# Performance work log

Hardware: AMD Instinct MI355X
Metric: run time of the kernel (lower is better)

## Reference

```python
import jax, jax.numpy as jnp
import numpy as np

NUM_HEADS = 16
KEY_DIM = 128
VALUE_DIM = 128
HIDDEN = 2048


def setup_inputs() -> dict:
    key = jax.random.key(0)
    k1, k2, k3 = jax.random.split(key, 3)
    B, T = 4, 2048
    hidden_states = jax.random.normal(k1, (B, T, HIDDEN), dtype=jnp.float32)
    # qkv_proj: Linear(hidden, H*(2*key_dim+value_dim)) no bias -> weight (out, in)
    qkv_out = NUM_HEADS * (2 * KEY_DIM + VALUE_DIM)
    w_qkv = jax.random.normal(k2, (qkv_out, HIDDEN), dtype=jnp.float32) * (1.0 / np.sqrt(HIDDEN))
    w_out = jax.random.normal(k3, (HIDDEN, NUM_HEADS * VALUE_DIM), dtype=jnp.float32) * (1.0 / np.sqrt(NUM_HEADS * VALUE_DIM))
    b_out = jnp.zeros((HIDDEN,), dtype=jnp.float32)
    return {"hidden_states": hidden_states, "w_qkv": w_qkv, "w_out": w_out, "b_out": b_out}


def reference(hidden_states, w_qkv, w_out, b_out):
    B, T, _ = hidden_states.shape
    H, Dk, Dv = NUM_HEADS, KEY_DIM, VALUE_DIM
    scale = 1.0 / np.sqrt(Dk).astype(np.float32)
    qkv = hidden_states @ w_qkv.T  # (B,T,H*(2Dk+Dv))
    q, k, v = jnp.split(qkv, [H * Dk, 2 * H * Dk], axis=-1)
    q = q.reshape(B, T, H, Dk).transpose(0, 2, 1, 3)  # (B,H,T,Dk)
    k = k.reshape(B, T, H, Dk).transpose(0, 2, 1, 3)
    v = v.reshape(B, T, H, Dv).transpose(0, 2, 1, 3)
    scores = jnp.einsum('bhtd,bhsd->bhts', q, k) * scale  # (B,H,T,S)
    causal = jnp.tril(jnp.ones((T, T), dtype=bool))
    scores = jnp.where(causal[None, None], scores, jnp.float32(-jnp.inf))
    attn = jax.nn.softmax(scores, axis=-1)
    out = jnp.einsum('bhts,bhsd->bhtd', attn, v)  # (B,H,T,Dv)
    out = out.transpose(0, 2, 1, 3).reshape(B, T, H * Dv)
    return out @ w_out.T + b_out
```

## Files before the change

### kernel.cpp

```cpp
#include <hip/hip_runtime.h>
#include <hip/hip_bf16.h>
#include <stdint.h>

#define HID   2048
#define NH    16
#define QKV_N 6144
#define BT    8192
#define TT    2048

typedef short bf16x8  __attribute__((ext_vector_type(8)));
typedef float f32x4   __attribute__((ext_vector_type(4)));
typedef float f32x16  __attribute__((ext_vector_type(16)));
typedef unsigned short u16;

__device__ __forceinline__ u16 f2bf(float f){
  union { float f; unsigned u; } v; v.f = f;
  unsigned r = 0x7fffu + ((v.u >> 16) & 1u);
  return (u16)((v.u + r) >> 16);
}
__device__ __forceinline__ float bf2f(u16 x){
  union { unsigned u; float f; } v; v.u = ((unsigned)x) << 16;
  return v.f;
}
__device__ __forceinline__ unsigned cvt_pk_bf16(float lo, float hi){
  unsigned r;
  asm("v_cvt_pk_bf16_f32 %0, %1, %2" : "=v"(r) : "v"(lo), "v"(hi));
  return r;
}

typedef __attribute__((address_space(3))) void lds_vt;
typedef const __attribute__((address_space(1))) void gbl_vt;

__device__ __forceinline__ void gload16(const void* g, void* l){
  __builtin_amdgcn_global_load_lds((gbl_vt*)g, (lds_vt*)l, 16, 0, 0);
}

#define FENCE() asm volatile("" ::: "memory")
#define SYNC()  { FENCE(); __builtin_amdgcn_s_barrier(); FENCE(); }

__global__ __launch_bounds__(256) void cvt_all(const float* __restrict__ in1, u16* __restrict__ o1, int n1,
                                               const float* __restrict__ in2, u16* __restrict__ o2, int n2,
                                               const float* __restrict__ in3, u16* __restrict__ o3, int n3){
  int i = blockIdx.x * blockDim.x + threadIdx.x;
  const int stride = gridDim.x * blockDim.x;
  const int ntot = n1 + n2 + n3;
  for (; i < ntot; i += stride){
    const float* ip; u16* op; int k;
    if (i < n1)            { ip = in1; op = o1; k = i; }
    else if (i < n1 + n2)  { ip = in2; op = o2; k = i - n1; }
    else                   { ip = in3; op = o3; k = i - n1 - n2; }
    float4 v = ((const float4*)ip)[k];
    ushort4 o;
    o.x = f2bf(v.x); o.y = f2bf(v.y); o.z = f2bf(v.z); o.w = f2bf(v.w);
    ((ushort4*)op)[k] = o;
  }
}

template<int OUT_BF16>
__global__ __launch_bounds__(512, 2) void gemm256(const u16* __restrict__ A,
                                                  const u16* __restrict__ Bm,
                                                  u16* __restrict__ Cb,
                                                  float* __restrict__ Cf,
                                                  const float* __restrict__ bias,
                                                  int M, int N, int K)
{
  __shared__ u16 lds[4 * 256 * 64];
  u16* const Abuf[2] = { lds,          lds + 16384 };
  u16* const Bbuf[2] = { lds + 32768,  lds + 49152 };

  const int tid  = threadIdx.x;
  const int w    = tid >> 6;
  const int lane = tid & 63;
  const int wm   = w >> 2;
  const int wn   = w & 3;
  const int lr   = lane & 15;
  const int lg   = lane >> 4;

  int bid = blockIdx.x;
  { int qq = gridDim.x >> 3; bid = (bid & 7) * qq + (bid >> 3); }
  const int ntile = N >> 8;
  const int m0 = (bid / ntile) << 8;
  const int n0 = (bid % ntile) << 8;

  const int rS = tid >> 3;
  const int cS = ((tid & 7) ^ (rS & 7)) * 8;
  const u16* gA = A  + (size_t)(m0 + rS) * K + cS;
  const u16* gB = Bm + (size_t)(n0 + rS) * K + cS;
  const int wds = w * 512;

  f32x4 acc[8][4] = {};
  bf16x8 aq[2][2], bq[4][2];

  auto stgA = [&](int buf, int half, int kt){
    const u16* s = gA + (size_t)(half * 128) * K + (size_t)kt * 64;
    gload16(s,                  Abuf[buf] + half * 8192 + wds);
    gload16(s + (size_t)64 * K, Abuf[buf] + half * 8192 + 4096 + wds);
  };
  auto stgB = [&](int buf, int half, int kt){
    const u16* s = gB + (size_t)(half * 128) * K + (size_t)kt * 64;
    gload16(s,                  Bbuf[buf] + half * 8192 + wds);
    gload16(s + (size_t)64 * K, Bbuf[buf] + half * 8192 + 4096 + wds);
  };
  auto loadA = [&](const u16* ab, int q){
    #pragma unroll
    for (int kk = 0; kk < 2; ++kk){
      #pragma unroll
      for (int mf2 = 0; mf2 < 2; ++mf2){
        int row = wm * 128 + (q * 2 + mf2) * 16 + lr;
        int blk = (kk * 4 + lg) ^ (lr & 7);
        aq[mf2][kk] = *(const bf16x8*)(ab + row * 64 + blk * 8);
      }
    }
  };
  auto loadB = [&](const u16* bb){
    #pragma unroll
    for (int nf = 0; nf < 4; ++nf){
      #pragma unroll
      for (int kk = 0; kk < 2; ++kk){
        int row = wn * 64 + nf * 16 + lr;
        int blk = (kk * 4 + lg) ^ (lr & 7);
        bq[nf][kk] = *(const bf16x8*)(bb + row * 64 + blk * 8);
      }
    }
  };

#define MFMAQ(Q) do {                                                         \
    __builtin_amdgcn_s_setprio(1);                                            \
    _Pragma("unroll")                                                         \
    for (int kk = 0; kk < 2; ++kk){                                           \
      _Pragma("unroll")                                                       \
      for (int mf2 = 0; mf2 < 2; ++mf2){                                      \
        _Pragma("unroll")                                                     \
        for (int nf = 0; nf < 4; ++nf)                                        \
          acc[(Q)*2+mf2][nf] = __builtin_amdgcn_mfma_f32_16x16x32_bf16(       \
              aq[mf2][kk], bq[nf][kk], acc[(Q)*2+mf2][nf], 0, 0, 0);          \
      }                                                                       \
    }                                                                         \
    __builtin_amdgcn_s_setprio(0);                                            \
  } while (0)

  stgA(0, 0, 0); stgA(0, 1, 0);
  stgB(0, 0, 0); stgB(0, 1, 0);
  stgB(1, 0, 1); stgB(1, 1, 1);
  asm volatile("s_waitcnt vmcnt(4)" ::: "memory");
  SYNC();

  const int NI = K >> 7;
  for (int it = 0; it < NI; ++it){
    const int t = it * 2;
    const bool lastI = (it == NI - 1);

    loadB(Bbuf[0]);
    loadA(Abuf[0], 0);
    stgA(1, 0, t + 1);
    SYNC(); MFMAQ(0); SYNC();

    loadA(Abuf[0], 1);
    stgA(1, 1, t + 1);
    SYNC(); MFMAQ(1); SYNC();

    loadA(Abuf[0], 2);
    if (!lastI) stgB(0, 0, t + 2);
    SYNC(); MFMAQ(2); SYNC();

    loadA(Abuf[0], 3);
    if (!lastI) stgB(0, 1, t + 2);
    SYNC(); MFMAQ(3);
    if (lastI) asm volatile("s_waitcnt vmcnt(0)" ::: "memory");
    else       asm volatile("s_waitcnt vmcnt(4)" ::: "memory");
    SYNC();

    loadB(Bbuf[1]);
    loadA(Abuf[1], 0);
    if (!lastI) stgA(0, 0, t + 2);
    SYNC(); MFMAQ(0); SYNC();

    loadA(Abuf[1], 1);
    if (!lastI) stgA(0, 1, t + 2);
    SYNC(); MFMAQ(1); SYNC();

    loadA(Abuf[1], 2);
    if (!lastI) stgB(1, 0, t + 3);
    SYNC(); MFMAQ(2); SYNC();

    loadA(Abuf[1], 3);
    if (!lastI) stgB(1, 1, t + 3);
    SYNC(); MFMAQ(3);
    if (!lastI) asm volatile("s_waitcnt vmcnt(4)" ::: "memory");
    SYNC();
  }
#undef MFMAQ

  const int orow = m0 + wm * 128 + lg * 4;
  const int ocol = n0 + wn * 64 + lr;
  #pragma unroll
  for (int mf = 0; mf < 8; ++mf)
    #pragma unroll
    for (int nf = 0; nf < 4; ++nf)
      #pragma unroll
      for (int r = 0; r < 4; ++r){
        int row = orow + mf * 16 + r;
        int col = ocol + nf * 16;
        float v = acc[mf][nf][r];
        if (OUT_BF16)
          Cb[(size_t)row * N + col] = f2bf(v);
        else
          Cf[(size_t)row * N + col] = v + bias[col];
      }
}

__global__ __launch_bounds__(256) void vtrans(const u16* __restrict__ qkv,
                                              u16* __restrict__ vt2){
  __shared__ u16 tile[32][136];
  const int t5 = blockIdx.x;
  const int bh = blockIdx.y;
  const int b = bh >> 4, h = bh & 15;
  const int tid = threadIdx.x;

  #pragma unroll
  for (int p = 0; p < 2; ++p){
    int idx = p * 256 + tid;
    int row = idx >> 4;
    int c8  = (idx & 15) * 8;
    bf16x8 v = *(const bf16x8*)(qkv + (size_t)(b * TT + t5 * 32 + row) * QKV_N + 4096 + h * 128 + c8);
    *(bf16x8*)(&tile[row][c8]) = v;
  }
  __syncthreads();
  u16* outp = vt2 + (size_t)(bh * 64 + t5) * 4096;
  #pragma unroll
  for (int p = 0; p < 2; ++p){
    int id = p * 256 + tid;
    int r  = id >> 3;
    int sp = id & 7;
    int sl = sp ^ (r & 7);
    int d  = (sl >> 2) * 64 + r;
    int kv = (sl & 3) * 8;
    bf16x8 v;
    #pragma unroll
    for (int e = 0; e < 8; ++e) v[e] = (short)tile[kv + e][d];
    *(bf16x8*)(outp + id * 8) = v;
  }
}

__global__ __launch_bounds__(256, 3) void attn(const u16* __restrict__ qkv,
                                               const u16* __restrict__ vt2,
                                               u16* __restrict__ aout)
{
  __shared__ u16 Kl[3][32 * 128];
  __shared__ u16 Vl[3][64 * 64];

  const int qt = 15 - (int)blockIdx.y;
  const int bh = blockIdx.x;
  const int b = bh >> 4, h = bh & 15;
  const int tid  = threadIdx.x;
  const int w    = tid >> 6;
  const int lane = tid & 63;
  const int l31  = lane & 31;
  const int hi   = lane >> 5;
  const int sw7  = l31 & 7;

  const int qg = qt * 128 + w * 32 + l31;
  const float sc2 = 0.08838834764831845f * 1.4426950408889634f;

  bf16x8 qf[8];
  {
    const u16* qp = qkv + (size_t)(b * TT + qg) * QKV_N + h * 128 + hi * 8;
    #pragma unroll
    for (int s = 0; s < 8; ++s){
      bf16x8 raw = *(const bf16x8*)(qp + s * 16);
      unsigned pk[4];
      #pragma unroll
      for (int p2 = 0; p2 < 4; ++p2)
        pk[p2] = cvt_pk_bf16(bf2f((u16)raw[2 * p2]) * sc2,
                             bf2f((u16)raw[2 * p2 + 1]) * sc2);
      int4 u = { (int)pk[0], (int)pk[1], (int)pk[2], (int)pk[3] };
      qf[s] = *(bf16x8*)&u;
    }
  }

  f32x16 o[4] = {};
  float lsum = 0.f;

  const u16* ksrc = qkv + (size_t)(b * TT + (tid >> 4)) * QKV_N + 2048 + h * 128
                    + (((tid & 15) ^ ((tid >> 4) & 7)) * 8);
  const u16* vsrc = vt2 + (size_t)bh * (64 * 4096) + tid * 8;

  auto stage = [&](int buf, int j){
    const u16* ks = ksrc + (size_t)(j * 32) * QKV_N;
    gload16(ks,                      &Kl[buf][tid * 8]);
    gload16(ks + (size_t)16 * QKV_N, &Kl[buf][2048 + tid * 8]);
    const u16* vs = vsrc + (size_t)j * 4096;
    gload16(vs,        &Vl[buf][tid * 8]);
    gload16(vs + 2048, &Vl[buf][2048 + tid * 8]);
  };

  const int NT  = 4 * qt + 4;
  const int jme = qt * 4 + w;
  stage(0, 0);
  stage(1, 1);

  int cur = 0;
  for (int j = 0; j < NT; ++j){
    SYNC();
    if (j + 2 < NT){
      int nb = cur + 2; if (nb >= 3) nb -= 3;
      stage(nb, j + 2);
      asm volatile("s_waitcnt vmcnt(8)" ::: "memory");
    } else if (j + 1 < NT){
      asm volatile("s_waitcnt vmcnt(4)" ::: "memory");
    } else {
      asm volatile("s_waitcnt vmcnt(0)" ::: "memory");
    }
    SYNC();

    if (j <= jme){
      f32x16 sa = {}, sb = {};
      const u16* KB = Kl[cur];
      __builtin_amdgcn_s_setprio(1);
      #pragma unroll
      for (int sl = 0; sl < 4; ++sl){
        const int spa = ((sl * 2 + hi) ^ sw7) * 8;
        const int spb = (((sl + 4) * 2 + hi) ^ sw7) * 8;
        bf16x8 ka = *(const bf16x8*)(KB + l31 * 128 + spa);
        bf16x8 kb2 = *(const bf16x8*)(KB + l31 * 128 + spb);
        sa = __builtin_amdgcn_mfma_f32_32x32x16_bf16(ka,  qf[sl],     sa, 0, 0, 0);
        sb = __builtin_amdgcn_mfma_f32_32x32x16_bf16(kb2, qf[sl + 4], sb, 0, 0, 0);
      }
      __builtin_amdgcn_s_setprio(0);

      f32x16 s;
      #pragma unroll
      for (int r = 0; r < 16; ++r) s[r] = sa[r] + sb[r];

      if (j == jme){
        #pragma unroll
        for (int r = 0; r < 16; ++r){
          const int krow = (r & 3) + 8 * (r >> 2) + 4 * hi;
          if (krow > l31) s[r] = -3.0e38f;
        }
      }

      #pragma unroll
      for (int r = 0; r < 16; ++r) s[r] = exp2f(s[r]);
      {
        float t0 = (s[0] + s[1]) + (s[2] + s[3]);
        float t1 = (s[4] + s[5]) + (s[6] + s[7]);
        float t2 = (s[8] + s[9]) + (s[10] + s[11]);
        float t3 = (s[12] + s[13]) + (s[14] + s[15]);
        lsum += (t0 + t1) + (t2 + t3);
      }

      bf16x8 pf[2];
      #pragma unroll
      for (int kb = 0; kb < 2; ++kb){
        const int R0 = kb * 8;
        const unsigned wa0 = cvt_pk_bf16(s[R0],     s[R0 + 1]);
        const unsigned wa1 = cvt_pk_bf16(s[R0 + 2], s[R0 + 3]);
        const unsigned wb0 = cvt_pk_bf16(s[R0 + 4], s[R0 + 5]);
        const unsigned wb1 = cvt_pk_bf16(s[R0 + 6], s[R0 + 7]);
        const int s0 = hi ? (int)wa0 : (int)wb0;
        const int s1 = hi ? (int)wa1 : (int)wb1;
        const int r0 = __shfl_xor(s0, 32, 64);
        const int r1 = __shfl_xor(s1, 32, 64);
        int4 u;
        u.x = hi ? r0 : (int)wa0;
        u.y = hi ? r1 : (int)wa1;
        u.z = hi ? (int)wb0 : r0;
        u.w = hi ? (int)wb1 : r1;
        pf[kb] = *(bf16x8*)&u;
      }

      const u16* VB = Vl[cur];
      __builtin_amdgcn_s_setprio(1);
      #pragma unroll
      for (int db = 0; db < 4; ++db){
        const int r6 = (db & 1) * 32 + l31;
        const int hd = db >> 1;
        #pragma unroll
        for (int kb = 0; kb < 2; ++kb){
          const int sp = ((hd * 4 + kb * 2 + hi) ^ sw7) * 8;
          bf16x8 vf = *(const bf16x8*)(VB + r6 * 64 + sp);
          o[db] = __builtin_amdgcn_mfma_f32_32x32x16_bf16(vf, pf[kb], o[db], 0, 0, 0);
        }
      }
      __builtin_amdgcn_s_setprio(0);
    }

    ++cur; if (cur == 3) cur = 0;
  }

  const float lt = lsum + __shfl_xor(lsum, 32, 64);
  const float inv = 1.0f / lt;
  u16* op = aout + (size_t)(b * TT + qg) * HID + h * 128;
  #pragma unroll
  for (int db = 0; db < 4; ++db)
    #pragma unroll
    for (int rq = 0; rq < 4; ++rq){
      ushort4 pk;
      pk.x = f2bf(o[db][rq * 4 + 0] * inv);
      pk.y = f2bf(o[db][rq * 4 + 1] * inv);
      pk.z = f2bf(o[db][rq * 4 + 2] * inv);
      pk.w = f2bf(o[db][rq * 4 + 3] * inv);
      *(ushort4*)(op + db * 32 + rq * 8 + hi * 4) = pk;
    }
}

extern "C" void kernel_launch(void* const* d_in, const int* in_sizes, int n_in,
                              void* d_out, int out_size, void* d_ws, size_t ws_size,
                              hipStream_t stream)
{
  (void)in_sizes; (void)n_in; (void)out_size; (void)ws_size;
  const float* hs    = (const float*)d_in[0];
  const float* w_qkv = (const float*)d_in[1];
  const float* w_out = (const float*)d_in[2];
  const float* b_out = (const float*)d_in[3];
  float* out = (float*)d_out;

  char* ws = (char*)d_ws;
  u16* qkv_bf  = (u16*)(ws);
  u16* wout_bf = (u16*)(ws + 100663296);
  u16* hs_bf   = (u16*)(ws + 109051904);
  u16* attn_bf = hs_bf;
  u16* wqkv_bf = (u16*)(ws + 142606336);
  u16* vt2_bf  = wqkv_bf;

  cvt_all<<<4096, 256, 0, stream>>>(hs,    hs_bf,   (BT * HID) / 4,
                                    w_qkv, wqkv_bf, (QKV_N * HID) / 4,
                                    w_out, wout_bf, (HID * 2048) / 4);

  gemm256<1><<<(BT / 256) * (QKV_N / 256), 512, 0, stream>>>(
      hs_bf, wqkv_bf, qkv_bf, nullptr, nullptr, BT, QKV_N, HID);

  vtrans<<<dim3(TT / 32, 64), 256, 0, stream>>>(qkv_bf, vt2_bf);

  attn<<<dim3(64, 16), 256, 0, stream>>>(qkv_bf, vt2_bf, attn_bf);

  gemm256<0><<<(BT / 256) * (HID / 256), 512, 0, stream>>>(
      attn_bf, wout_bf, nullptr, out, b_out, BT, HID, HID);
}
```

Baseline: 371.9 us.

## Fuse V transpose into QKV GEMM epilogue, dropping separate vtrans kernel

The QKV GEMM epilogue now writes the V columns straight into the swizzled transposed vt2 layout used by attention. Q and K are stored in a narrower buffer with row pitch 4096. This removes the vtrans launch along with its read and write pass over V, and it shrinks the qkv buffer. In exchange, the V-tile epilogue does scattered 2-byte stores, which may coalesce poorly.

```diff
diff --git a/kernel.cpp b/kernel.cpp
--- a/kernel.cpp
+++ b/kernel.cpp
@@ -5,6 +5,7 @@
 #define HID   2048
 #define NH    16
 #define QKV_N 6144
+#define QKP   4096
 #define BT    8192
 #define TT    2048
 
@@ -56,12 +57,13 @@
   }
 }
 
-template<int OUT_BF16>
+template<int MODE>
 __global__ __launch_bounds__(512, 2) void gemm256(const u16* __restrict__ A,
                                                   const u16* __restrict__ Bm,
                                                   u16* __restrict__ Cb,
                                                   float* __restrict__ Cf,
                                                   const float* __restrict__ bias,
+                                                  u16* __restrict__ vt2,
                                                   int M, int N, int K)
 {
   __shared__ u16 lds[4 * 256 * 64];
@@ -193,56 +195,49 @@
 
   const int orow = m0 + wm * 128 + lg * 4;
   const int ocol = n0 + wn * 64 + lr;
-  #pragma unroll
-  for (int mf = 0; mf < 8; ++mf)
-    #pragma unroll
-    for (int nf = 0; nf < 4; ++nf)
-      #pragma unroll
-      for (int r = 0; r < 4; ++r){
-        int row = orow + mf * 16 + r;
-        int col = ocol + nf * 16;
-        float v = acc[mf][nf][r];
-        if (OUT_BF16)
-          Cb[(size_t)row * N + col] = f2bf(v);
-        else
-          Cf[(size_t)row * N + col] = v + bias[col];
-      }
-}
-
-__global__ __launch_bounds__(256) void vtrans(const u16* __restrict__ qkv,
-                                              u16* __restrict__ vt2){
-  __shared__ u16 tile[32][136];
-  const int t5 = blockIdx.x;
-  const int bh = blockIdx.y;
-  const int b = bh >> 4, h = bh & 15;
-  const int tid = threadIdx.x;
-
-  #pragma unroll
-  for (int p = 0; p < 2; ++p){
-    int idx = p * 256 + tid;
-    int row = idx >> 4;
-    int c8  = (idx & 15) * 8;
-    bf16x8 v = *(const bf16x8*)(qkv + (size_t)(b * TT + t5 * 32 + row) * QKV_N + 4096 + h * 128 + c8);
-    *(bf16x8*)(&tile[row][c8]) = v;
+
+  if (MODE == 1 && n0 >= 4096){
+    #pragma unroll
+    for (int nf = 0; nf < 4; ++nf){
+      const int c   = ocol + nf * 16 - 4096;
+      const int h2  = c >> 7;
+      const int d   = c & 127;
+      const int r64 = d & 63;
+      const int hd  = d >> 6;
+      #pragma unroll
+      for (int mf = 0; mf < 8; ++mf)
+        #pragma unroll
+        for (int r = 0; r < 4; ++r){
+          const int row = orow + mf * 16 + r;
+          const int bb  = row >> 11;
+          const int t   = row & 2047;
+          const int t5  = t >> 5;
+          const int kv  = t & 31;
+          const int sl  = hd * 4 + (kv >> 3);
+          const int sp  = sl ^ (r64 & 7);
+          vt2[(size_t)((bb * 16 + h2) * 64 + t5) * 4096 + r64 * 64 + sp * 8 + (kv & 7)]
+              = f2bf(acc[mf][nf][r]);
+        }
+    }
+  } else {
+    #pragma unroll
+    for (int mf = 0; mf < 8; ++mf)
+      #pragma unroll
+      for (int nf = 0; nf < 4; ++nf)
+        #pragma unroll
+        for (int r = 0; r < 4; ++r){
+          int row = orow + mf * 16 + r;
+          int col = ocol + nf * 16;
+          float v = acc[mf][nf][r];
+          if (MODE == 1)
+            Cb[(size_t)row * QKP + col] = f2bf(v);
+          else
+            Cf[(size_t)row * N + col] = v + bias[col];
+        }
   }
-  __syncthreads();
-  u16* outp = vt2 + (size_t)(bh * 64 + t5) * 4096;
-  #pragma unroll
-  for (int p = 0; p < 2; ++p){
-    int id = p * 256 + tid;
-    int r  = id >> 3;
-    int sp = id & 7;
-    int sl = sp ^ (r & 7);
-    int d  = (sl >> 2) * 64 + r;
-    int kv = (sl & 3) * 8;
-    bf16x8 v;
-    #pragma unroll
-    for (int e = 0; e < 8; ++e) v[e] = (short)tile[kv + e][d];
-    *(bf16x8*)(outp + id * 8) = v;
-  }
-}
-
-__global__ __launch_bounds__(256, 3) void attn(const u16* __restrict__ qkv,
+}
+
+__global__ __launch_bounds__(256, 3) void attn(const u16* __restrict__ qk,
                                                const u16* __restrict__ vt2,
                                                u16* __restrict__ aout)
 {
@@ -264,7 +259,7 @@
 
   bf16x8 qf[8];
   {
-    const u16* qp = qkv + (size_t)(b * TT + qg) * QKV_N + h * 128 + hi * 8;
+    const u16* qp = qk + (size_t)(b * TT + qg) * QKP + h * 128 + hi * 8;
     #pragma unroll
     for (int s = 0; s < 8; ++s){
       bf16x8 raw = *(const bf16x8*)(qp + s * 16);
@@ -281,14 +276,14 @@
   f32x16 o[4] = {};
   float lsum = 0.f;
 
-  const u16* ksrc = qkv + (size_t)(b * TT + (tid >> 4)) * QKV_N + 2048 + h * 128
+  const u16* ksrc = qk + (size_t)(b * TT + (tid >> 4)) * QKP + 2048 + h * 128
                     + (((tid & 15) ^ ((tid >> 4) & 7)) * 8);
   const u16* vsrc = vt2 + (size_t)bh * (64 * 4096) + tid * 8;
 
   auto stage = [&](int buf, int j){
-    const u16* ks = ksrc + (size_t)(j * 32) * QKV_N;
-    gload16(ks,                      &Kl[buf][tid * 8]);
-    gload16(ks + (size_t)16 * QKV_N, &Kl[buf][2048 + tid * 8]);
+    const u16* ks = ksrc + (size_t)(j * 32) * QKP;
+    gload16(ks,                    &Kl[buf][tid * 8]);
+    gload16(ks + (size_t)16 * QKP, &Kl[buf][2048 + tid * 8]);
     const u16* vs = vsrc + (size_t)j * 4096;
     gload16(vs,        &Vl[buf][tid * 8]);
     gload16(vs + 2048, &Vl[buf][2048 + tid * 8]);
@@ -417,24 +412,22 @@
   float* out = (float*)d_out;
 
   char* ws = (char*)d_ws;
-  u16* qkv_bf  = (u16*)(ws);
+  u16* qk_bf   = (u16*)(ws);
+  u16* vt2_bf  = (u16*)(ws + 67108864);
   u16* wout_bf = (u16*)(ws + 100663296);
   u16* hs_bf   = (u16*)(ws + 109051904);
   u16* attn_bf = hs_bf;
   u16* wqkv_bf = (u16*)(ws + 142606336);
-  u16* vt2_bf  = wqkv_bf;
 
   cvt_all<<<4096, 256, 0, stream>>>(hs,    hs_bf,   (BT * HID) / 4,
                                     w_qkv, wqkv_bf, (QKV_N * HID) / 4,
                                     w_out, wout_bf, (HID * 2048) / 4);
 
   gemm256<1><<<(BT / 256) * (QKV_N / 256), 512, 0, stream>>>(
-      hs_bf, wqkv_bf, qkv_bf, nullptr, nullptr, BT, QKV_N, HID);
-
-  vtrans<<<dim3(TT / 32, 64), 256, 0, stream>>>(qkv_bf, vt2_bf);
-
-  attn<<<dim3(64, 16), 256, 0, stream>>>(qkv_bf, vt2_bf, attn_bf);
+      hs_bf, wqkv_bf, qk_bf, nullptr, nullptr, vt2_bf, BT, QKV_N, HID);
+
+  attn<<<dim3(64, 16), 256, 0, stream>>>(qk_bf, vt2_bf, attn_bf);
 
   gemm256<0><<<(BT / 256) * (HID / 256), 512, 0, stream>>>(
-      attn_bf, wout_bf, nullptr, out, b_out, BT, HID, HID);
-}
+      attn_bf, wout_bf, nullptr, out, b_out, nullptr, BT, HID, HID);
+}
```

Measured after the change: 362.6 us (median of 2 runs). 2.5% less time.
